# Performance work log

Measured on AMD Instinct MI355X. Metric: run time of the kernel, lower is better.

The kernel has to match this reference:

```python
import jax, jax.numpy as jnp
import numpy as np

B, FIN, H, W = 16, 256, 32, 32
NH, FH = 8, 64
CIN = FIN + 2  # fin + 2 coordinate-grid pos channels
COUT = NH * FH


def setup_inputs() -> dict:
    key = jax.random.key(0)
    ks = jax.random.split(key, 9)
    s = 1.0 / np.sqrt(CIN)
    so = 1.0 / np.sqrt(COUT)
    return {
        "x": jax.random.normal(ks[0], (B, FIN, H, W), dtype=jnp.float32),
        "wq": jax.random.uniform(ks[1], (COUT, CIN), jnp.float32, -s, s),
        "bq": jax.random.uniform(ks[2], (COUT,), jnp.float32, -s, s),
        "wk": jax.random.uniform(ks[3], (COUT, CIN), jnp.float32, -s, s),
        "bk": jax.random.uniform(ks[4], (COUT,), jnp.float32, -s, s),
        "wv": jax.random.uniform(ks[5], (COUT, CIN), jnp.float32, -s, s),
        "bv": jax.random.uniform(ks[6], (COUT,), jnp.float32, -s, s),
        "wo": jax.random.uniform(ks[7], (FIN, COUT), jnp.float32, -so, so),
        "bo": jax.random.uniform(ks[8], (FIN,), jnp.float32, -so, so),
    }


def reference(x, wq, bq, wk, bk, wv, bv, wo, bo):
    b, c, h, w = x.shape
    n = h * w
    # PosEncoding: concat one linspace(-1,1) coordinate channel per spatial dim
    gy, gx = jnp.meshgrid(jnp.linspace(-1.0, 1.0, h), jnp.linspace(-1.0, 1.0, w), indexing="ij")
    pos = jnp.broadcast_to(jnp.stack([gy, gx])[None], (b, 2, h, w)).astype(x.dtype)
    t = jnp.concatenate([x, pos], axis=1).reshape(b, c + 2, n)  # [B, C+2, N]
    # 1x1 convs are per-token GEMMs
    q = (jnp.einsum("oc,bcn->bon", wq, t) + bq[:, None]).reshape(b, NH, FH, n)
    k = (jnp.einsum("oc,bcn->bon", wk, t) + bk[:, None]).reshape(b, NH, FH, n)
    v = (jnp.einsum("oc,bcn->bon", wv, t) + bv[:, None]).reshape(b, NH, FH, n)
    temp = FH ** 0.5
    attn = jax.nn.softmax(jnp.einsum("bhdn,bhdm->bhnm", q, k) / temp, axis=-1)
    o = jnp.einsum("bhnm,bhdm->bhdn", attn, v).reshape(b, NH * FH, n)
    o = jnp.einsum("oc,bcn->bon", wo, o) + bo[:, None]
    return x + o.reshape(b, c, h, w)
```

## Files before the change

kernel.cpp:

```cpp
#include <hip/hip_runtime.h>


typedef unsigned short u16;
typedef unsigned int   u32;
typedef __attribute__((ext_vector_type(8))) short  short8;
typedef __attribute__((ext_vector_type(4))) float  float4_;

#define MFMA16(a, b, c) __builtin_amdgcn_mfma_f32_16x16x32_bf16(a, b, c, 0, 0, 0)

__device__ __forceinline__ float bf2f(u16 u) {
    union { u32 i; float f; } v; v.i = ((u32)u) << 16; return v.f;
}
__device__ __forceinline__ u16 f2bf(float f) {
    union { float f; u32 i; } v; v.f = f;
    u32 r = v.i + 0x7FFFu + ((v.i >> 16) & 1u);
    return (u16)(r >> 16);
}
__device__ __forceinline__ float exp2_fast(float x) {
    float r;
    asm("v_exp_f32 %0, %1" : "=v"(r) : "v"(x));
    return r;
}
__device__ __forceinline__ u32 cvtpk_bf16(float lo, float hi) {
    u32 r;
    asm("v_cvt_pk_bf16_f32 %0, %1, %2" : "=v"(r) : "v"(lo), "v"(hi));
    return r;
}
__device__ __forceinline__ void pl32swap(u32 &x, u32 &y) {
    asm volatile("v_permlane32_swap_b32 %0, %1" : "+v"(x), "+v"(y));
}
__device__ __forceinline__ void pl16swap(u32 &x, u32 &y) {
    asm volatile("v_permlane16_swap_b32 %0, %1" : "+v"(x), "+v"(y));
}

__global__ __launch_bounds__(256) void prep(
    const float* __restrict__ wq, const float* __restrict__ wk,
    const float* __restrict__ wv, const float* __restrict__ x,
    u16* __restrict__ wb, u16* __restrict__ xT)
{
    __shared__ float Lt[64][65];
    const int bid = blockIdx.x;
    const int tid = threadIdx.x;
    if (bid < 512) {
        int i = bid * 256 + tid;
        int o = i >> 8, c = i & 255;
        size_t si = (size_t)o * 258 + c;
        wb[i]          = f2bf(wq[si]);
        wb[131072 + i] = f2bf(wk[si]);
        wb[262144 + i] = f2bf(wv[si]);
    } else {
        int r = bid - 512;
        int n0 = (r & 15) * 64, c0 = ((r >> 4) & 3) * 64, b = r >> 6;
#pragma unroll
        for (int p = 0; p < 4; ++p) {
            int c = p * 16 + (tid >> 4);
            int nn = (tid & 15) * 4;
            float4 v = *(const float4*)&x[((size_t)(b * 256) + c0 + c) * 1024 + n0 + nn];
            Lt[c][nn + 0] = v.x; Lt[c][nn + 1] = v.y;
            Lt[c][nn + 2] = v.z; Lt[c][nn + 3] = v.w;
        }
        __syncthreads();
#pragma unroll
        for (int p = 0; p < 4; ++p) {
            int n = p * 16 + (tid >> 4);
            int cc = (tid & 15) * 4;
            ushort4 st;
            st.x = f2bf(Lt[cc + 0][n]); st.y = f2bf(Lt[cc + 1][n]);
            st.z = f2bf(Lt[cc + 2][n]); st.w = f2bf(Lt[cc + 3][n]);
            *(ushort4*)&xT[((size_t)(b << 10) + n0 + n) * 256 + c0 + cc] = st;
        }
    }
}

__global__ __launch_bounds__(256) void qkv_mfma(
    const u16* __restrict__ xT, const u16* __restrict__ wb,
    const float* __restrict__ wq, const float* __restrict__ wk,
    const float* __restrict__ wv,
    const float* __restrict__ bq, const float* __restrict__ bk,
    const float* __restrict__ bv,
    u16* __restrict__ qkvbuf)
{
    __shared__ u16 Wl[128 * 64];
    __shared__ u16 Tl[128 * 64];
    const int tid = threadIdx.x;
    const int lane = tid & 63, w = tid >> 6;
    const int quad = lane >> 4, m15 = lane & 15;
    const int n0 = blockIdx.x * 128, mt = blockIdx.y, b = blockIdx.z;
    const int mat = mt >> 2;
    const int m0 = mt * 128;
    const float* worig = (mat == 0) ? wq : ((mat == 1) ? wk : wv);
    const float* bias  = (mat == 0) ? bq : ((mat == 1) ? bk : bv);
    const float oscale = (mat == 1) ? 0.1803368801111204f : 1.0f;
    u16* outbuf = qkvbuf + (size_t)mat * 8388608;

    float4_ acc[2][8];
#pragma unroll
    for (int s = 0; s < 2; ++s)
#pragma unroll
        for (int t = 0; t < 8; ++t) acc[s][t] = (float4_){0, 0, 0, 0};

    const int srow = tid >> 2;
    const int sc8  = (tid & 3) * 8;
    const int rdsw = (m15 & 7) << 3;
    const int sw0  = (srow & 7) << 3;

    const u16* wsrc = wb + (size_t)(m0 + srow) * 256 + sc8;
    const u16* tsrc = xT + ((size_t)(b << 10) + n0 + srow) * 256 + sc8;

    {
        short8 w0 = *(const short8*)(wsrc);
        short8 w1 = *(const short8*)(wsrc + 64 * 256);
        short8 t0 = *(const short8*)(tsrc);
        short8 t1 = *(const short8*)(tsrc + 64 * 256);
        *(short8*)&Wl[srow * 64 + (sc8 ^ sw0)]        = w0;
        *(short8*)&Wl[(srow + 64) * 64 + (sc8 ^ sw0)] = w1;
        *(short8*)&Tl[srow * 64 + (sc8 ^ sw0)]        = t0;
        *(short8*)&Tl[(srow + 64) * 64 + (sc8 ^ sw0)] = t1;
    }
    __syncthreads();

#pragma unroll
    for (int k = 0; k < 8; ++k) {
        const int p = k & 1;
        short8 pw0, pw1, pt0, pt1;
        if (k < 7) {
            const int kc = (k + 1) * 32;
            pw0 = *(const short8*)(wsrc + kc);
            pw1 = *(const short8*)(wsrc + 64 * 256 + kc);
            pt0 = *(const short8*)(tsrc + kc);
            pt1 = *(const short8*)(tsrc + 64 * 256 + kc);
        }

        const int cb = p * 32 + quad * 8;
        short8 af0 = *(const short8*)&Wl[(w * 32 + m15) * 64 + (cb ^ rdsw)];
        short8 af1 = *(const short8*)&Wl[(w * 32 + 16 + m15) * 64 + (cb ^ rdsw)];
        __builtin_amdgcn_s_setprio(1);
#pragma unroll
        for (int t = 0; t < 8; ++t) {
            short8 bf = *(const short8*)&Tl[(t * 16 + m15) * 64 + (cb ^ rdsw)];
            acc[0][t] = MFMA16(af0, bf, acc[0][t]);
            acc[1][t] = MFMA16(af1, bf, acc[1][t]);
        }
        __builtin_amdgcn_s_setprio(0);

        if (k < 7) {
            const int pc = (p ^ 1) * 32 + sc8;
            *(short8*)&Wl[srow * 64 + (pc ^ sw0)]        = pw0;
            *(short8*)&Wl[(srow + 64) * 64 + (pc ^ sw0)] = pw1;
            *(short8*)&Tl[srow * 64 + (pc ^ sw0)]        = pt0;
            *(short8*)&Tl[(srow + 64) * 64 + (pc ^ sw0)] = pt1;
        }
        __syncthreads();
    }

#pragma unroll
    for (int s = 0; s < 2; ++s) {
        float wg[4], wx[4], bi[4];
#pragma unroll
        for (int r = 0; r < 4; ++r) {
            int om = (mt & 3) * 128 + w * 32 + s * 16 + quad * 4 + r;
            wg[r] = worig[(size_t)om * 258 + 256];
            wx[r] = worig[(size_t)om * 258 + 257];
            bi[r] = bias[om];
        }
        const int h = (mt & 3) * 2 + ((w * 32 + s * 16) >> 6);
        const int dbase = ((w * 32 + s * 16) & 63) + quad * 4;
#pragma unroll
        for (int t = 0; t < 8; ++t) {
            int n = n0 + t * 16 + m15;
            float gy = -1.0f + 2.0f * (float)(n >> 5) / 31.0f;
            float gx = -1.0f + 2.0f * (float)(n & 31) / 31.0f;
            float v[4];
#pragma unroll
            for (int r = 0; r < 4; ++r)
                v[r] = (acc[s][t][r] + wg[r] * gy + wx[r] * gx + bi[r]) * oscale;
            if (mat != 2) {
                ushort4 st;
                st.x = f2bf(v[0]); st.y = f2bf(v[1]);
                st.z = f2bf(v[2]); st.w = f2bf(v[3]);
                *(ushort4*)&outbuf[((size_t)(b * 8 + h) * 1024 + n) * 64 + dbase] = st;
            } else {
#pragma unroll
                for (int r = 0; r < 4; ++r)
                    outbuf[((size_t)(b * 8 + h) * 64 + dbase + r) * 1024 + n] = f2bf(v[r]);
            }
        }
    }
}

__global__ __launch_bounds__(512) void attn_mfma(
    u16* __restrict__ qbuf, const u16* __restrict__ kbuf,
    const u16* __restrict__ vbuf)
{
    __shared__ u16 Kl[64 * 64];
    __shared__ u16 Vl[64 * 64];

    const int tid = threadIdx.x;
    const int lane = tid & 63, w = tid >> 6;
    const int quad = lane >> 4, m15 = lane & 15;
    const int bh = blockIdx.x;
    const int q0 = blockIdx.y * 256;
    u16* qb = qbuf + (size_t)bh * 65536;
    const u16* kb = kbuf + (size_t)bh * 65536;
    const u16* vb = vbuf + (size_t)bh * 65536;

    short8 qf[2][2];
#pragma unroll
    for (int s = 0; s < 2; ++s) {
        const u16* qr = qb + (size_t)(q0 + w * 32 + s * 16 + m15) * 64 + quad * 8;
        qf[s][0] = *(const short8*)qr;
        qf[s][1] = *(const short8*)(qr + 32);
    }

    float4_ O[2][4];
    float lp[2] = {0.0f, 0.0f};
#pragma unroll
    for (int s = 0; s < 2; ++s)
#pragma unroll
        for (int t = 0; t < 4; ++t) O[s][t] = (float4_){0, 0, 0, 0};

    const int row = tid >> 3, c8 = (tid & 7) * 8;
    const int stsw = c8 ^ ((row & 7) << 3);
    const int rdsw = (m15 & 7) << 3;

    for (int kt0 = 0; kt0 < 1024; kt0 += 64) {
        __syncthreads();
        *(short8*)&Kl[row * 64 + stsw] =
            *(const short8*)(kb + (size_t)(kt0 + row) * 64 + c8);
        *(short8*)&Vl[row * 64 + stsw] =
            *(const short8*)(vb + (size_t)row * 1024 + kt0 + c8);
        __syncthreads();

        float4_ S[2][4];
#pragma unroll
        for (int s = 0; s < 2; ++s)
#pragma unroll
            for (int t = 0; t < 4; ++t) S[s][t] = (float4_){0, 0, 0, 0};
#pragma unroll
        for (int c = 0; c < 2; ++c) {
            short8 kf[4];
#pragma unroll
            for (int t = 0; t < 4; ++t)
                kf[t] = *(const short8*)&Kl[(t * 16 + m15) * 64 +
                                            ((c * 32 + quad * 8) ^ rdsw)];
            __builtin_amdgcn_s_setprio(1);
#pragma unroll
            for (int s = 0; s < 2; ++s)
#pragma unroll
                for (int t = 0; t < 4; ++t)
                    S[s][t] = MFMA16(kf[t], qf[s][c], S[s][t]);
            __builtin_amdgcn_s_setprio(0);
        }

        u32 W0[2][4], W1[2][4];
#pragma unroll
        for (int s = 0; s < 2; ++s) {
            float lsum = 0.0f;
#pragma unroll
            for (int t = 0; t < 4; ++t) {
                float p0 = exp2_fast(S[s][t][0]);
                float p1 = exp2_fast(S[s][t][1]);
                float p2 = exp2_fast(S[s][t][2]);
                float p3 = exp2_fast(S[s][t][3]);
                W0[s][t] = cvtpk_bf16(p0, p1);
                W1[s][t] = cvtpk_bf16(p2, p3);
                lsum += (p0 + p1) + (p2 + p3);
            }
            lp[s] += lsum;
        }

#pragma unroll
        for (int c = 0; c < 2; ++c) {
            short8 av[4];
#pragma unroll
            for (int dt = 0; dt < 4; ++dt)
                av[dt] = *(const short8*)&Vl[(dt * 16 + m15) * 64 +
                                             ((c * 32 + quad * 8) ^ rdsw)];
#pragma unroll
            for (int s = 0; s < 2; ++s) {
                u32 a = W0[s][2 * c], d = W0[s][2 * c + 1];
                pl32swap(a, d); pl16swap(a, d);
                u32 bb = W1[s][2 * c], e = W1[s][2 * c + 1];
                pl32swap(bb, e); pl16swap(bb, e);
                union { u32 u[4]; short8 v; } bpu;
                bpu.u[0] = a; bpu.u[1] = bb; bpu.u[2] = d; bpu.u[3] = e;
                short8 bp = bpu.v;
                __builtin_amdgcn_s_setprio(1);
#pragma unroll
                for (int dt = 0; dt < 4; ++dt)
                    O[s][dt] = MFMA16(av[dt], bp, O[s][dt]);
                __builtin_amdgcn_s_setprio(0);
            }
        }
    }

#pragma unroll
    for (int s = 0; s < 2; ++s) {
        float v = lp[s];
        v += __shfl_xor(v, 16);
        v += __shfl_xor(v, 32);
        float linv = 1.0f / v;
        int n = q0 + w * 32 + s * 16 + m15;
#pragma unroll
        for (int dt = 0; dt < 4; ++dt) {
            ushort4 st;
            st.x = f2bf(O[s][dt][0] * linv);
            st.y = f2bf(O[s][dt][1] * linv);
            st.z = f2bf(O[s][dt][2] * linv);
            st.w = f2bf(O[s][dt][3] * linv);
            *(ushort4*)&qb[(size_t)n * 64 + dt * 16 + quad * 4] = st;
        }
    }
}

__global__ __launch_bounds__(256) void proj_mfma(
    const u16* __restrict__ ao, const float* __restrict__ wo,
    const float* __restrict__ bo, const float* __restrict__ x,
    float* __restrict__ out)
{
    __shared__ u16 Wl[64 * 64];
    __shared__ u16 Tl[64 * 64];
    const int tid = threadIdx.x;
    const int lane = tid & 63, w = tid >> 6;
    const int quad = lane >> 4, m15 = lane & 15;
    const int n0 = blockIdx.x * 64, f0 = blockIdx.y * 64, b = blockIdx.z;

    float4_ acc[4] = {{0,0,0,0},{0,0,0,0},{0,0,0,0},{0,0,0,0}};
    const int srow = tid >> 2;
    const int sc8  = (tid & 3) * 8;
    const int sw0  = (srow & 7) << 3;
    const int rdsw = (m15 & 7) << 3;

    const float* wsrc = wo + (size_t)(f0 + srow) * 512 + sc8;
    const u16* tbase = ao + ((size_t)(b << 3) * 1024 + n0 + srow) * 64 + sc8;

    {
        float4 v0 = *(const float4*)(wsrc);
        float4 v1 = *(const float4*)(wsrc + 4);
        uint4 pk;
        pk.x = cvtpk_bf16(v0.x, v0.y); pk.y = cvtpk_bf16(v0.z, v0.w);
        pk.z = cvtpk_bf16(v1.x, v1.y); pk.w = cvtpk_bf16(v1.z, v1.w);
        *(uint4*)&Wl[srow * 64 + (sc8 ^ sw0)] = pk;
        *(short8*)&Tl[srow * 64 + (sc8 ^ sw0)] = *(const short8*)(tbase);
    }
    __syncthreads();

#pragma unroll
    for (int k = 0; k < 16; ++k) {
        const int p = k & 1;
        float4 pv0, pv1; short8 pt;
        if (k < 15) {
            const int kc = (k + 1) * 32;
            pv0 = *(const float4*)(wsrc + kc);
            pv1 = *(const float4*)(wsrc + kc + 4);
            pt  = *(const short8*)(tbase + (size_t)(kc >> 6) * 65536 + (kc & 63));
        }

        const int cb = p * 32 + quad * 8;
        short8 af = *(const short8*)&Wl[(w * 16 + m15) * 64 + (cb ^ rdsw)];
        __builtin_amdgcn_s_setprio(1);
#pragma unroll
        for (int t = 0; t < 4; ++t) {
            short8 bf = *(const short8*)&Tl[(t * 16 + m15) * 64 + (cb ^ rdsw)];
            acc[t] = MFMA16(af, bf, acc[t]);
        }
        __builtin_amdgcn_s_setprio(0);

        if (k < 15) {
            const int pc = ((p ^ 1) * 32 + sc8) ^ sw0;
            uint4 pk;
            pk.x = cvtpk_bf16(pv0.x, pv0.y); pk.y = cvtpk_bf16(pv0.z, pv0.w);
            pk.z = cvtpk_bf16(pv1.x, pv1.y); pk.w = cvtpk_bf16(pv1.z, pv1.w);
            *(uint4*)&Wl[srow * 64 + pc] = pk;
            *(short8*)&Tl[srow * 64 + pc] = pt;
        }
        __syncthreads();
    }

    float bi[4];
#pragma unroll
    for (int r = 0; r < 4; ++r) bi[r] = bo[f0 + w * 16 + quad * 4 + r];
#pragma unroll
    for (int t = 0; t < 4; ++t) {
        int n = n0 + t * 16 + m15;
#pragma unroll
        for (int r = 0; r < 4; ++r) {
            int f = f0 + w * 16 + quad * 4 + r;
            size_t idx = ((size_t)(b * 256) + f) * 1024 + n;
            out[idx] = acc[t][r] + bi[r] + x[idx];
        }
    }
}

extern "C" void kernel_launch(void* const* d_in, const int* in_sizes, int n_in,
                              void* d_out, int out_size, void* d_ws, size_t ws_size,
                              hipStream_t stream) {
    const float* x  = (const float*)d_in[0];
    const float* wq = (const float*)d_in[1];
    const float* bq = (const float*)d_in[2];
    const float* wk = (const float*)d_in[3];
    const float* bk = (const float*)d_in[4];
    const float* wv = (const float*)d_in[5];
    const float* bv = (const float*)d_in[6];
    const float* wo = (const float*)d_in[7];
    const float* bo = (const float*)d_in[8];

    u16* qkvbuf = (u16*)d_ws;
    u16* region = qkvbuf + 3 * 8388608;
    u16* xT = region;
    u16* wb = region + 4194304;

    prep<<<1536, 256, 0, stream>>>(wq, wk, wv, x, wb, xT);

    qkv_mfma<<<dim3(8, 12, 16), 256, 0, stream>>>(
        xT, wb, wq, wk, wv, bq, bk, bv, qkvbuf);

    attn_mfma<<<dim3(128, 4), 512, 0, stream>>>(
        qkvbuf, qkvbuf + 8388608, qkvbuf + 16777216);

    proj_mfma<<<dim3(16, 4, 16), 256, 0, stream>>>(qkvbuf, wo, bo, x, (float*)d_out);
}
```

Baseline: 166.6 us.

## Double QKV GEMM M-tile to 256 rows with 512-thread blocks

The QKV projection kernel now computes a 256x128 output tile per block using 8 waves instead of a 128x128 tile with 4 waves, halving the grid's y dimension. Each X^T tile loaded into shared memory is therefore reused across twice as many weight rows, cutting global loads of the activation operand. The trade-off is more shared memory per block (48 KB), larger blocks and fewer blocks overall, which may lower occupancy and tail balance.

```diff
diff --git a/kernel.cpp b/kernel.cpp
--- a/kernel.cpp
+++ b/kernel.cpp
@@ -72,7 +72,7 @@
     }
 }
 
-__global__ __launch_bounds__(256) void qkv_mfma(
+__global__ __launch_bounds__(512) void qkv_mfma(
     const u16* __restrict__ xT, const u16* __restrict__ wb,
     const float* __restrict__ wq, const float* __restrict__ wk,
     const float* __restrict__ wv,
@@ -80,14 +80,14 @@
     const float* __restrict__ bv,
     u16* __restrict__ qkvbuf)
 {
-    __shared__ u16 Wl[128 * 64];
+    __shared__ u16 Wl[256 * 64];
     __shared__ u16 Tl[128 * 64];
     const int tid = threadIdx.x;
     const int lane = tid & 63, w = tid >> 6;
     const int quad = lane >> 4, m15 = lane & 15;
-    const int n0 = blockIdx.x * 128, mt = blockIdx.y, b = blockIdx.z;
-    const int mat = mt >> 2;
-    const int m0 = mt * 128;
+    const int n0 = blockIdx.x * 128, mt2 = blockIdx.y, b = blockIdx.z;
+    const int mat = mt2 >> 1;
+    const int m0 = mt2 * 256;
     const float* worig = (mat == 0) ? wq : ((mat == 1) ? wk : wv);
     const float* bias  = (mat == 0) ? bq : ((mat == 1) ? bk : bv);
     const float oscale = (mat == 1) ? 0.1803368801111204f : 1.0f;
@@ -99,36 +99,34 @@
 #pragma unroll
         for (int t = 0; t < 8; ++t) acc[s][t] = (float4_){0, 0, 0, 0};
 
-    const int srow = tid >> 2;
-    const int sc8  = (tid & 3) * 8;
+    const int srw = tid >> 2;
+    const int sc8 = (tid & 3) * 8;
     const int rdsw = (m15 & 7) << 3;
-    const int sw0  = (srow & 7) << 3;
-
-    const u16* wsrc = wb + (size_t)(m0 + srow) * 256 + sc8;
-    const u16* tsrc = xT + ((size_t)(b << 10) + n0 + srow) * 256 + sc8;
+    const int sw0  = (srw & 7) << 3;
+
+    const u16* wsrc  = wb + (size_t)(m0 + srw) * 256 + sc8;
+    const u16* wsrc2 = wsrc + (size_t)128 * 256;
+    const u16* tsrc  = xT + ((size_t)(b << 10) + n0 + srw) * 256 + sc8;
 
     {
         short8 w0 = *(const short8*)(wsrc);
-        short8 w1 = *(const short8*)(wsrc + 64 * 256);
+        short8 w1 = *(const short8*)(wsrc2);
         short8 t0 = *(const short8*)(tsrc);
-        short8 t1 = *(const short8*)(tsrc + 64 * 256);
-        *(short8*)&Wl[srow * 64 + (sc8 ^ sw0)]        = w0;
-        *(short8*)&Wl[(srow + 64) * 64 + (sc8 ^ sw0)] = w1;
-        *(short8*)&Tl[srow * 64 + (sc8 ^ sw0)]        = t0;
-        *(short8*)&Tl[(srow + 64) * 64 + (sc8 ^ sw0)] = t1;
+        *(short8*)&Wl[srw * 64 + (sc8 ^ sw0)]         = w0;
+        *(short8*)&Wl[(srw + 128) * 64 + (sc8 ^ sw0)] = w1;
+        *(short8*)&Tl[srw * 64 + (sc8 ^ sw0)]         = t0;
     }
     __syncthreads();
 
 #pragma unroll
     for (int k = 0; k < 8; ++k) {
         const int p = k & 1;
-        short8 pw0, pw1, pt0, pt1;
+        short8 pw0, pw1, pt0;
         if (k < 7) {
             const int kc = (k + 1) * 32;
             pw0 = *(const short8*)(wsrc + kc);
-            pw1 = *(const short8*)(wsrc + 64 * 256 + kc);
+            pw1 = *(const short8*)(wsrc2 + kc);
             pt0 = *(const short8*)(tsrc + kc);
-            pt1 = *(const short8*)(tsrc + 64 * 256 + kc);
         }
 
         const int cb = p * 32 + quad * 8;
@@ -145,26 +143,26 @@
 
         if (k < 7) {
             const int pc = (p ^ 1) * 32 + sc8;
-            *(short8*)&Wl[srow * 64 + (pc ^ sw0)]        = pw0;
-            *(short8*)&Wl[(srow + 64) * 64 + (pc ^ sw0)] = pw1;
-            *(short8*)&Tl[srow * 64 + (pc ^ sw0)]        = pt0;
-            *(short8*)&Tl[(srow + 64) * 64 + (pc ^ sw0)] = pt1;
+            *(short8*)&Wl[srw * 64 + (pc ^ sw0)]         = pw0;
+            *(short8*)&Wl[(srw + 128) * 64 + (pc ^ sw0)] = pw1;
+            *(short8*)&Tl[srw * 64 + (pc ^ sw0)]         = pt0;
         }
         __syncthreads();
     }
 
 #pragma unroll
     for (int s = 0; s < 2; ++s) {
+        const int om_base = (mt2 & 1) * 256 + w * 32 + s * 16;
         float wg[4], wx[4], bi[4];
 #pragma unroll
         for (int r = 0; r < 4; ++r) {
-            int om = (mt & 3) * 128 + w * 32 + s * 16 + quad * 4 + r;
+            int om = om_base + quad * 4 + r;
             wg[r] = worig[(size_t)om * 258 + 256];
             wx[r] = worig[(size_t)om * 258 + 257];
             bi[r] = bias[om];
         }
-        const int h = (mt & 3) * 2 + ((w * 32 + s * 16) >> 6);
-        const int dbase = ((w * 32 + s * 16) & 63) + quad * 4;
+        const int h = om_base >> 6;
+        const int dbase = (om_base & 63) + quad * 4;
 #pragma unroll
         for (int t = 0; t < 8; ++t) {
             int n = n0 + t * 16 + m15;
@@ -412,7 +410,7 @@
 
     prep<<<1536, 256, 0, stream>>>(wq, wk, wv, x, wb, xT);
 
-    qkv_mfma<<<dim3(8, 12, 16), 256, 0, stream>>>(
+    qkv_mfma<<<dim3(8, 6, 16), 512, 0, stream>>>(
         xT, wb, wq, wk, wv, bq, bk, bv, qkvbuf);
 
     attn_mfma<<<dim3(128, 4), 512, 0, stream>>>(
```

Result: no change. 167.8 us (+0.7%).
